# Kernel tuning notes

Measured on AMD Instinct MI355X. Metric: run time of the kernel, lower is better.

Reference implementation:

```python
import jax, jax.numpy as jnp
import numpy as np

DECAY = 0.1
EPS = 1e-5


def setup_inputs() -> dict:
    key = jax.random.key(0)
    k1, k2, k3, k4 = jax.random.split(key, 4)
    N, K, D = 262144, 1024, 64
    x = jax.random.normal(k1, (N, D), dtype=jnp.float32)
    embed = jax.random.normal(k2, (K, D), dtype=jnp.float32) * 0.01
    cluster_size = jax.random.uniform(k3, (K,), dtype=jnp.float32)
    embed_avg = jax.random.normal(k4, (K, D), dtype=jnp.float32) * 0.01
    return {"x": x, "embed": embed, "cluster_size": cluster_size, "embed_avg": embed_avg}


def reference(x, embed, cluster_size, embed_avg):
    # x: [N, D] flattened latents; embed: [K, D] codebook
    N, D = x.shape
    K = embed.shape[0]

    # Squared Euclidean distance (same argmin as torch.cdist p=2).
    x2 = jnp.sum(x * x, axis=-1, keepdims=True)            # [N, 1]
    e2 = jnp.sum(embed * embed, axis=-1)                   # [K]
    dist = x2 - 2.0 * jnp.einsum('nd,kd->nk', x, embed) + e2[None, :]  # [N, K]
    embed_ind = jnp.argmin(dist, axis=-1)                  # [N] int

    # Quantize: gather nearest codes.
    quantize = embed[embed_ind]                            # [N, D]

    # --- EMA codebook update (no-grad in the original) ---
    xs = jax.lax.stop_gradient(x)
    bins = jax.ops.segment_sum(jnp.ones((N,), dtype=x.dtype), embed_ind,
                               num_segments=K)             # [K] bincount
    embed_sum = jax.ops.segment_sum(xs, embed_ind, num_segments=K)  # [K, D] scatter-add

    cluster_size_new = cluster_size * DECAY + bins * (1.0 - DECAY)
    embed_avg_new = embed_avg * DECAY + embed_sum * (1.0 - DECAY)

    # Laplace smoothing then normalize to get the updated codebook.
    n = jnp.sum(cluster_size_new)
    cs_smoothed = (cluster_size_new + EPS) / (n + K * EPS) * n
    embed_normalized = embed_avg_new / cs_smoothed[:, None]  # [K, D]

    return quantize, embed_ind, cluster_size_new, embed_avg_new, embed_normalized
```

## Files before the change

### kernel.cpp

```cpp
#include <hip/hip_runtime.h>
#include <hip/hip_bf16.h>


#define NROWS 262144
#define KCODES 1024
#define DDIM 64
#define CAPL 4

typedef __attribute__((ext_vector_type(8))) short short8;
typedef __attribute__((ext_vector_type(4))) float f32x4;

__device__ __forceinline__ unsigned short f2bf(float f) {
    unsigned u = __float_as_uint(f);
    unsigned r = u + 0x7fffu + ((u >> 16) & 1u);
    return (unsigned short)(r >> 16);
}

__global__ __launch_bounds__(256) void vq_prep(
    const float* __restrict__ embed, unsigned short* __restrict__ eb,
    float* __restrict__ e2f, float* __restrict__ enmax2)
{
    const int k = blockIdx.x * 256 + threadIdx.x;
    const float* er = embed + (size_t)k * DDIM;
    float s = 0.f;
    #pragma unroll
    for (int d = 0; d < DDIM; ++d) { float v = er[d]; s = fmaf(v, v, s); }
    e2f[k] = s;
    unsigned char* base = (unsigned char*)eb + (k >> 8) * 32768 +
                          ((k >> 5) & 7) * 4096 + (k & 31) * 128;
    #pragma unroll
    for (int sl = 0; sl < 8; ++sl) {
        short8 f;
        #pragma unroll
        for (int j = 0; j < 8; ++j) f[j] = (short)f2bf(er[sl * 8 + j]);
        *reinterpret_cast<short8*>(base + ((sl ^ (k & 7)) << 4)) = f;
    }
    atomicMax((int*)enmax2, __float_as_int(s));
}

__global__ __launch_bounds__(512) void vq_phaseA(
    const float* __restrict__ x, const unsigned short* __restrict__ eb,
    const float* __restrict__ e2f, const float* __restrict__ enmax2,
    float* __restrict__ out_ind, int* __restrict__ candg, int* __restrict__ cntg,
    int* __restrict__ wl, int* __restrict__ gcount,
    int* __restrict__ wl2, int* __restrict__ gcount2, int* __restrict__ bins_i)
{
    __shared__ __align__(16) unsigned short ebs0[16384];
    __shared__ __align__(16) unsigned short ebs1[16384];
    __shared__ float e2L[KCODES];
    __shared__ float norm2L[256];
    __shared__ int   cntL[256];
    __shared__ int   candL[256][CAPL];
    __shared__ int   mcount, mbase, mcount2, mbase2;

    const int t    = threadIdx.x;
    const int lane = t & 63;
    const int wid  = t >> 6;
    const int col  = lane & 15;
    const int q    = lane >> 4;
    const int rowb = blockIdx.x * 256;
    const int r0   = wid * 32;

#define STAGEQ(BUF, P)                                                        \
    {                                                                         \
        const unsigned char* gsrc = (const unsigned char*)eb +                \
            (size_t)(P) * 32768 + t * 16;                                     \
        unsigned char* ldst = (unsigned char*)(BUF) + t * 16;                 \
        _Pragma("unroll")                                                     \
        for (int it = 0; it < 4; ++it)                                        \
            __builtin_amdgcn_global_load_lds(                                 \
                (const __attribute__((address_space(1))) void*)(gsrc + it * 8192), \
                (__attribute__((address_space(3))) void*)(ldst + it * 8192),  \
                16, 0, 0);                                                    \
    }

    STAGEQ(ebs0, 0)

    short8 a0[2], a1[2];
    {
        const float* xr = x + (size_t)(rowb + r0 + col) * DDIM;
        float s = 0.f;
        #pragma unroll
        for (int m = 0; m < 2; ++m) {
            const float4 u = *reinterpret_cast<const float4*>(xr + m * 32 + 8 * q);
            const float4 v = *reinterpret_cast<const float4*>(xr + m * 32 + 8 * q + 4);
            short8 f;
            f[0] = (short)f2bf(u.x); f[1] = (short)f2bf(u.y);
            f[2] = (short)f2bf(u.z); f[3] = (short)f2bf(u.w);
            f[4] = (short)f2bf(v.x); f[5] = (short)f2bf(v.y);
            f[6] = (short)f2bf(v.z); f[7] = (short)f2bf(v.w);
            a0[m] = f;
            s = fmaf(u.x, u.x, s); s = fmaf(u.y, u.y, s);
            s = fmaf(u.z, u.z, s); s = fmaf(u.w, u.w, s);
            s = fmaf(v.x, v.x, s); s = fmaf(v.y, v.y, s);
            s = fmaf(v.z, v.z, s); s = fmaf(v.w, v.w, s);
        }
        s += __shfl_xor(s, 16); s += __shfl_xor(s, 32);
        if (lane < 16) norm2L[r0 + lane] = s;
    }
    {
        const float* xr = x + (size_t)(rowb + r0 + 16 + col) * DDIM;
        float s = 0.f;
        #pragma unroll
        for (int m = 0; m < 2; ++m) {
            const float4 u = *reinterpret_cast<const float4*>(xr + m * 32 + 8 * q);
            const float4 v = *reinterpret_cast<const float4*>(xr + m * 32 + 8 * q + 4);
            short8 f;
            f[0] = (short)f2bf(u.x); f[1] = (short)f2bf(u.y);
            f[2] = (short)f2bf(u.z); f[3] = (short)f2bf(u.w);
            f[4] = (short)f2bf(v.x); f[5] = (short)f2bf(v.y);
            f[6] = (short)f2bf(v.z); f[7] = (short)f2bf(v.w);
            a1[m] = f;
            s = fmaf(u.x, u.x, s); s = fmaf(u.y, u.y, s);
            s = fmaf(u.z, u.z, s); s = fmaf(u.w, u.w, s);
            s = fmaf(v.x, v.x, s); s = fmaf(v.y, v.y, s);
            s = fmaf(v.z, v.z, s); s = fmaf(v.w, v.w, s);
        }
        s += __shfl_xor(s, 16); s += __shfl_xor(s, 32);
        if (lane < 16) norm2L[r0 + 16 + lane] = s;
    }

    e2L[t]       = -0.5f * e2f[t];
    e2L[512 + t] = -0.5f * e2f[512 + t];
    if (t < 256) cntL[t] = 0;
    if (t == 0) { mcount = 0; mcount2 = 0; }
    const float en2 = *enmax2;

    const int off0 = col * 128 + ((q       ^ (col & 7)) << 4);
    const int off1 = col * 128 + (((4 + q) ^ (col & 7)) << 4);

    f32x4 best0, best1;
    #pragma unroll
    for (int r = 0; r < 4; ++r) { best0[r] = -3.4e38f; best1[r] = -3.4e38f; }

#define CHUNKS(BUF, P, KIND)                                                  \
    _Pragma("unroll")                                                         \
    for (int ch = 0; ch < 16; ++ch) {                                         \
        const short8 b0 = *reinterpret_cast<const short8*>(                   \
            (char*)(BUF) + ch * 2048 + off0);                                 \
        const short8 b1 = *reinterpret_cast<const short8*>(                   \
            (char*)(BUF) + ch * 2048 + off1);                                 \
        const float e2n = e2L[(P) * 256 + ch * 16 + col];                     \
        f32x4 acc0, acc1;                                                     \
        acc0[0] = e2n; acc0[1] = e2n; acc0[2] = e2n; acc0[3] = e2n;           \
        acc1 = acc0;                                                          \
        acc0 = __builtin_amdgcn_mfma_f32_16x16x32_bf16(a0[0], b0, acc0, 0, 0, 0); \
        acc1 = __builtin_amdgcn_mfma_f32_16x16x32_bf16(a1[0], b0, acc1, 0, 0, 0); \
        acc0 = __builtin_amdgcn_mfma_f32_16x16x32_bf16(a0[1], b1, acc0, 0, 0, 0); \
        acc1 = __builtin_amdgcn_mfma_f32_16x16x32_bf16(a1[1], b1, acc1, 0, 0, 0); \
        if (KIND == 0) {                                                      \
            _Pragma("unroll")                                                 \
            for (int r = 0; r < 4; ++r) {                                     \
                best0[r] = fmaxf(best0[r], acc0[r]);                          \
                best1[r] = fmaxf(best1[r], acc1[r]);                          \
            }                                                                 \
        } else {                                                              \
            _Pragma("unroll")                                                 \
            for (int r = 0; r < 4; ++r) {                                     \
                if (acc0[r] >= best0[r]) {                                    \
                    const int rl = r0 + q * 4 + r;                            \
                    const int idx = atomicAdd(&cntL[rl], 1);                  \
                    if (idx < CAPL) candL[rl][idx] = (P) * 256 + ch * 16 + col; \
                }                                                             \
                if (acc1[r] >= best1[r]) {                                    \
                    const int rl = r0 + 16 + q * 4 + r;                       \
                    const int idx = atomicAdd(&cntL[rl], 1);                  \
                    if (idx < CAPL) candL[rl][idx] = (P) * 256 + ch * 16 + col; \
                }                                                             \
            }                                                                 \
        }                                                                     \
    }

    __syncthreads();
    STAGEQ(ebs1, 1)  CHUNKS(ebs0, 0, 0)  __syncthreads();
    STAGEQ(ebs0, 2)  CHUNKS(ebs1, 1, 0)  __syncthreads();
    STAGEQ(ebs1, 3)  CHUNKS(ebs0, 2, 0)  __syncthreads();
    CHUNKS(ebs1, 3, 0)

    #pragma unroll
    for (int r = 0; r < 4; ++r) {
        float v0 = best0[r], v1 = best1[r];
        v0 = fmaxf(v0, __shfl_xor(v0, 1));  v1 = fmaxf(v1, __shfl_xor(v1, 1));
        v0 = fmaxf(v0, __shfl_xor(v0, 2));  v1 = fmaxf(v1, __shfl_xor(v1, 2));
        v0 = fmaxf(v0, __shfl_xor(v0, 4));  v1 = fmaxf(v1, __shfl_xor(v1, 4));
        v0 = fmaxf(v0, __shfl_xor(v0, 8));  v1 = fmaxf(v1, __shfl_xor(v1, 8));
        const int lr = q * 4 + r;
        const float m0 = 0.0078125f * sqrtf(norm2L[r0 + lr] * en2) + 5e-5f;
        const float m1 = 0.0078125f * sqrtf(norm2L[r0 + 16 + lr] * en2) + 5e-5f;
        best0[r] = v0 - m0;
        best1[r] = v1 - m1;
    }

    STAGEQ(ebs0, 0)  CHUNKS(ebs1, 3, 1)  __syncthreads();
    STAGEQ(ebs1, 1)  CHUNKS(ebs0, 0, 1)  __syncthreads();
    STAGEQ(ebs0, 2)  CHUNKS(ebs1, 1, 1)  __syncthreads();
    CHUNKS(ebs0, 2, 1)
    __syncthreads();

    int my = -1, my2 = -1, c = 0;
    if (t < 256) {
        c = cntL[t];
        if (c == 1) {
            const int code = candL[t][0];
            out_ind[rowb + t] = (float)code;
            atomicAdd(bins_i + code, 1);
        }
        else if (c <= CAPL)   my  = atomicAdd(&mcount, 1);
        else                  my2 = atomicAdd(&mcount2, 1);
    }
    __syncthreads();
    if (t == 0) { mbase = atomicAdd(gcount, mcount); mbase2 = atomicAdd(gcount2, mcount2); }
    __syncthreads();
    if (my >= 0) {
        const int row = rowb + t;
        wl[mbase + my] = row;
        cntg[row] = c;
        #pragma unroll
        for (int j = 0; j < CAPL; ++j)
            if (j < c) candg[row * CAPL + j] = candL[t][j];
    }
    if (my2 >= 0) wl2[mbase2 + my2] = rowb + t;
#undef STAGEQ
#undef CHUNKS
}

__global__ __launch_bounds__(256) void vq_rerank(
    const float* __restrict__ x, const float* __restrict__ embed,
    const float* __restrict__ e2f, const int* __restrict__ wl,
    const int* __restrict__ gcount, const int* __restrict__ cntg,
    const int* __restrict__ candg, const int* __restrict__ wl2,
    const int* __restrict__ gcount2, float* __restrict__ out_ind,
    int* __restrict__ bins_i)
{
    const int t = threadIdx.x;
    const int n = *gcount;
    for (int i = blockIdx.x * 256 + t; i < n; i += gridDim.x * 256) {
        const int row = wl[i];
        float xv[DDIM];
        {
            const float4* xp = reinterpret_cast<const float4*>(x + (size_t)row * DDIM);
            float4 xq[16];
            #pragma unroll
            for (int qq = 0; qq < 16; ++qq) xq[qq] = xp[qq];
            #pragma unroll
            for (int qq = 0; qq < 16; ++qq) {
                xv[qq*4+0] = xq[qq].x; xv[qq*4+1] = xq[qq].y;
                xv[qq*4+2] = xq[qq].z; xv[qq*4+3] = xq[qq].w;
            }
        }
        float x2 = 0.f;
        #pragma unroll
        for (int d = 0; d < DDIM; ++d) x2 = fmaf(xv[d], xv[d], x2);

        const int c = cntg[row];
        float bv = 3.4e38f; int bk = 0x7fffffff;
        for (int ci = 0; ci < c; ++ci) {
            const int k = candg[row * CAPL + ci];
            const float4* ep = reinterpret_cast<const float4*>(embed + (size_t)k * DDIM);
            float dot = 0.f;
            #pragma unroll
            for (int qq = 0; qq < 16; ++qq) {
                const float4 e4 = ep[qq];
                dot = fmaf(xv[qq*4+0], e4.x, dot);
                dot = fmaf(xv[qq*4+1], e4.y, dot);
                dot = fmaf(xv[qq*4+2], e4.z, dot);
                dot = fmaf(xv[qq*4+3], e4.w, dot);
            }
            const float dist = (x2 - 2.0f * dot) + e2f[k];
            if (dist < bv || (dist == bv && k < bk)) { bv = dist; bk = k; }
        }
        out_ind[row] = (float)bk;
        atomicAdd(bins_i + bk, 1);
    }

    const int lane = t & 63;
    const int gw   = (blockIdx.x * 256 + t) >> 6;
    const int nw   = (gridDim.x * 256) >> 6;
    const int n2   = *gcount2;
    for (int e = gw; e < n2; e += nw) {
        const int row = wl2[e];
        float xv[DDIM];
        {
            const float4* xp = reinterpret_cast<const float4*>(x + (size_t)row * DDIM);
            #pragma unroll
            for (int qq = 0; qq < 16; ++qq) {
                const float4 v = xp[qq];
                xv[qq*4+0] = v.x; xv[qq*4+1] = v.y; xv[qq*4+2] = v.z; xv[qq*4+3] = v.w;
            }
        }
        float x2 = 0.f;
        #pragma unroll
        for (int d = 0; d < DDIM; ++d) x2 = fmaf(xv[d], xv[d], x2);

        float bv = 3.4e38f; int bk = 0x7fffffff;
        for (int k = lane; k < KCODES; k += 64) {
            const float* er = embed + (size_t)k * DDIM;
            float dot = 0.f;
            #pragma unroll
            for (int d = 0; d < DDIM; ++d) dot = fmaf(xv[d], er[d], dot);
            const float dist = (x2 - 2.0f * dot) + e2f[k];
            if (dist < bv) { bv = dist; bk = k; }
        }
        #pragma unroll
        for (int s = 1; s < 64; s <<= 1) {
            const float ov = __shfl_xor(bv, s);
            const int   ok = __shfl_xor(bk, s);
            if (ov < bv || (ov == bv && ok < bk)) { bv = ov; bk = ok; }
        }
        if (lane == 0) { out_ind[row] = (float)bk; atomicAdd(bins_i + bk, 1); }
    }
}

__global__ __launch_bounds__(1024) void vq_prefix(
    const int* __restrict__ bins_i, int* __restrict__ cursor)
{
    __shared__ int s[KCODES];
    const int t = threadIdx.x;
    const int b = bins_i[t];
    s[t] = b;
    __syncthreads();
    for (int d = 1; d < KCODES; d <<= 1) {
        const int v = (t >= d) ? s[t - d] : 0;
        __syncthreads();
        s[t] += v;
        __syncthreads();
    }
    cursor[t] = s[t] - b;
}

__global__ __launch_bounds__(256) void vq_scatter(
    const float* __restrict__ out_ind, int* __restrict__ cursor, int* __restrict__ sorted)
{
    const int row  = blockIdx.x * 256 + threadIdx.x;
    const int code = (int)out_ind[row];
    const int pos  = atomicAdd(cursor + code, 1);
    sorted[pos] = (code << 20) | row;
}

__global__ __launch_bounds__(256) void vq_reduce(
    const float* __restrict__ x, const int* __restrict__ sorted,
    float* __restrict__ esum)
{
    const int t = threadIdx.x, lane = t & 63, w = t >> 6;
    const int p0 = (blockIdx.x * 4 + w) * 64;

    int cur = sorted[p0] >> 20;
    float acc = 0.f;
    #pragma unroll 4
    for (int i = 0; i < 64; i += 4) {
        const int4 e4 = *reinterpret_cast<const int4*>(sorted + p0 + i);
        const float v0 = x[(size_t)(e4.x & 0xFFFFF) * DDIM + lane];
        const float v1 = x[(size_t)(e4.y & 0xFFFFF) * DDIM + lane];
        const float v2 = x[(size_t)(e4.z & 0xFFFFF) * DDIM + lane];
        const float v3 = x[(size_t)(e4.w & 0xFFFFF) * DDIM + lane];
        const int c0 = e4.x >> 20, c1 = e4.y >> 20, c2 = e4.z >> 20, c3 = e4.w >> 20;
        if (c0 != cur) { unsafeAtomicAdd(esum + cur * DDIM + lane, acc); acc = 0.f; cur = c0; }
        acc += v0;
        if (c1 != cur) { unsafeAtomicAdd(esum + cur * DDIM + lane, acc); acc = 0.f; cur = c1; }
        acc += v1;
        if (c2 != cur) { unsafeAtomicAdd(esum + cur * DDIM + lane, acc); acc = 0.f; cur = c2; }
        acc += v2;
        if (c3 != cur) { unsafeAtomicAdd(esum + cur * DDIM + lane, acc); acc = 0.f; cur = c3; }
        acc += v3;
    }
    unsafeAtomicAdd(esum + cur * DDIM + lane, acc);
}

__global__ __launch_bounds__(1024) void vq_finalize(
    const float* __restrict__ cluster_size, const float* __restrict__ embed_avg,
    const int* __restrict__ bins_i, float* __restrict__ out_cs,
    float* __restrict__ out_eavg, float* __restrict__ out_enorm)
{
    __shared__ float red[KCODES];
    __shared__ float css[KCODES];
    const int t = threadIdx.x;

    const float csn = cluster_size[t] * 0.1f + (float)bins_i[t] * 0.9f;
    red[t] = csn;
    __syncthreads();
    for (int s = 512; s > 0; s >>= 1) {
        if (t < s) red[t] += red[t + s];
        __syncthreads();
    }
    const float n = red[0];
    out_cs[t] = csn;
    css[t] = (csn + 1e-5f) / (n + (float)(KCODES * 1e-5)) * n;
    __syncthreads();

    #pragma unroll
    for (int i = 0; i < 16; ++i) {
        const int f4 = t + i * 1024;
        const int k  = f4 >> 4;
        const float4 ea = reinterpret_cast<const float4*>(embed_avg)[f4];
        const float4 su = reinterpret_cast<const float4*>(out_eavg)[f4];
        const float  cc = css[k];
        float4 ean, en;
        ean.x = ea.x * 0.1f + su.x * 0.9f; en.x = ean.x / cc;
        ean.y = ea.y * 0.1f + su.y * 0.9f; en.y = ean.y / cc;
        ean.z = ea.z * 0.1f + su.z * 0.9f; en.z = ean.z / cc;
        ean.w = ea.w * 0.1f + su.w * 0.9f; en.w = ean.w / cc;
        reinterpret_cast<float4*>(out_eavg)[f4]  = ean;
        reinterpret_cast<float4*>(out_enorm)[f4] = en;
    }
}

__global__ __launch_bounds__(256) void vq_quant(
    const float* __restrict__ out_ind, const float* __restrict__ embed,
    float* __restrict__ out_q)
{
    __shared__ int inds[256];
    const int t = threadIdx.x;
    const int row0 = blockIdx.x * 256;
    inds[t] = (int)out_ind[row0 + t];
    __syncthreads();
    #pragma unroll
    for (int i = 0; i < 16; ++i) {
        const int f = t + i * 256;
        const int r = f >> 4, dq = f & 15;
        const int code = inds[r];
        const float4 ev = *reinterpret_cast<const float4*>(
            embed + (size_t)code * DDIM + dq * 4);
        *reinterpret_cast<float4*>(out_q + (size_t)(row0 + r) * DDIM + dq * 4) = ev;
    }
}

extern "C" void kernel_launch(void* const* d_in, const int* in_sizes, int n_in,
                              void* d_out, int out_size, void* d_ws, size_t ws_size,
                              hipStream_t stream)
{
    const float* x            = (const float*)d_in[0];
    const float* embed        = (const float*)d_in[1];
    const float* cluster_size = (const float*)d_in[2];
    const float* embed_avg    = (const float*)d_in[3];

    float* out      = (float*)d_out;
    float* out_q    = out;
    float* out_ind  = out_q + (size_t)NROWS * DDIM;
    float* out_cs   = out_ind + NROWS;
    float* out_eavg = out_cs + KCODES;
    float* out_en   = out_eavg + (size_t)KCODES * DDIM;

    unsigned short* eb = (unsigned short*)out_en;
    float* e2f = out_en + 32768;

    int* S      = (int*)out_q;
    int* candg  = S;
    int* cntg   = S + 1048576;
    int* wl     = S + 1310720;
    int* wl2    = S + 1572864;
    int* sorted = S + 1835008;
    int* bins_i = S + 2097152;
    int* gcount = bins_i + KCODES;
    int* gcount2= gcount + 1;
    float* enmax2 = (float*)(gcount2 + 1);
    int* cursor = gcount2 + 2;

    hipMemsetAsync(bins_i, 0, (KCODES + 3) * sizeof(int), stream);
    hipMemsetAsync(out_eavg, 0, (size_t)KCODES * DDIM * sizeof(float), stream);

    vq_prep    <<<KCODES / 256, 256, 0, stream>>>(embed, eb, e2f, enmax2);
    vq_phaseA  <<<NROWS / 256, 512, 0, stream>>>(x, eb, e2f, enmax2, out_ind,
                                                 candg, cntg, wl, gcount,
                                                 wl2, gcount2, bins_i);
    vq_rerank  <<<512, 256, 0, stream>>>(x, embed, e2f, wl, gcount, cntg, candg,
                                         wl2, gcount2, out_ind, bins_i);
    vq_prefix  <<<1, 1024, 0, stream>>>(bins_i, cursor);
    vq_scatter <<<NROWS / 256, 256, 0, stream>>>(out_ind, cursor, sorted);
    vq_reduce  <<<NROWS / 256, 256, 0, stream>>>(x, sorted, out_eavg);
    vq_finalize<<<1, 1024, 0, stream>>>(cluster_size, embed_avg, bins_i,
                                        out_cs, out_eavg, out_en);
    vq_quant   <<<NROWS / 256, 256, 0, stream>>>(out_ind, embed, out_q);
}
```

Baseline: 304.0 us.

## Replace two-pass candidate collection with single-pass running top-3 tracking

The MFMA distance scan no longer makes a second full pass over the codebook to gather near-best candidates. Each lane now keeps a running top-3 (values) with top-2 indices, merges them across lanes with shuffles, and classifies each row as resolved, a two-candidate rerank, or a full fallback. This halves the MFMA and LDS staging work in phase A and simplifies the rerank kernel to exactly two candidates. In exchange it adds per-element select logic and extra registers for the top-3 state, which may lower occupancy, and rows whose third value is within the margin take the full fallback path.

```diff
diff --git a/kernel.cpp b/kernel.cpp
--- a/kernel.cpp
+++ b/kernel.cpp
@@ -5,10 +5,10 @@
 #define NROWS 262144
 #define KCODES 1024
 #define DDIM 64
-#define CAPL 4
 
 typedef __attribute__((ext_vector_type(8))) short short8;
 typedef __attribute__((ext_vector_type(4))) float f32x4;
+typedef __attribute__((ext_vector_type(4))) int   i32x4;
 
 __device__ __forceinline__ unsigned short f2bf(float f) {
     unsigned u = __float_as_uint(f);
@@ -38,10 +38,22 @@
     atomicMax((int*)enmax2, __float_as_int(s));
 }
 
+#define T3U(v, idx, V1, I1, V2, I2, V3)                                       \
+    {                                                                         \
+        const bool g1 = (v) > (V1);                                           \
+        const bool g2 = (v) > (V2);                                           \
+        const bool g3 = (v) > (V3);                                           \
+        (V3) = g2 ? (V2) : (g3 ? (v) : (V3));                                 \
+        (V2) = g1 ? (V1) : (g2 ? (v) : (V2));                                 \
+        (I2) = g1 ? (I1) : (g2 ? (idx) : (I2));                               \
+        (V1) = g1 ? (v) : (V1);                                               \
+        (I1) = g1 ? (idx) : (I1);                                             \
+    }
+
 __global__ __launch_bounds__(512) void vq_phaseA(
     const float* __restrict__ x, const unsigned short* __restrict__ eb,
     const float* __restrict__ e2f, const float* __restrict__ enmax2,
-    float* __restrict__ out_ind, int* __restrict__ candg, int* __restrict__ cntg,
+    float* __restrict__ out_ind, int* __restrict__ candg,
     int* __restrict__ wl, int* __restrict__ gcount,
     int* __restrict__ wl2, int* __restrict__ gcount2, int* __restrict__ bins_i)
 {
@@ -50,7 +62,7 @@
     __shared__ float e2L[KCODES];
     __shared__ float norm2L[256];
     __shared__ int   cntL[256];
-    __shared__ int   candL[256][CAPL];
+    __shared__ int   candL[256][2];
     __shared__ int   mcount, mbase, mcount2, mbase2;
 
     const int t    = threadIdx.x;
@@ -122,19 +134,23 @@
 
     e2L[t]       = -0.5f * e2f[t];
     e2L[512 + t] = -0.5f * e2f[512 + t];
-    if (t < 256) cntL[t] = 0;
     if (t == 0) { mcount = 0; mcount2 = 0; }
     const float en2 = *enmax2;
 
     const int off0 = col * 128 + ((q       ^ (col & 7)) << 4);
     const int off1 = col * 128 + (((4 + q) ^ (col & 7)) << 4);
 
-    f32x4 best0, best1;
-    #pragma unroll
-    for (int r = 0; r < 4; ++r) { best0[r] = -3.4e38f; best1[r] = -3.4e38f; }
-
-#define CHUNKS(BUF, P, KIND)                                                  \
-    _Pragma("unroll")                                                         \
+    f32x4 v1a, v2a, v3a, v1b, v2b, v3b;
+    i32x4 i1a, i2a, i1b, i2b;
+    #pragma unroll
+    for (int r = 0; r < 4; ++r) {
+        v1a[r] = -3.4e38f; v2a[r] = -3.4e38f; v3a[r] = -3.4e38f;
+        v1b[r] = -3.4e38f; v2b[r] = -3.4e38f; v3b[r] = -3.4e38f;
+        i1a[r] = 0; i2a[r] = 0; i1b[r] = 0; i2b[r] = 0;
+    }
+
+#define CHUNKS(BUF, P)                                                        \
+    _Pragma("unroll 4")                                                       \
     for (int ch = 0; ch < 16; ++ch) {                                         \
         const short8 b0 = *reinterpret_cast<const short8*>(                   \
             (char*)(BUF) + ch * 2048 + off0);                                 \
@@ -148,65 +164,69 @@
         acc1 = __builtin_amdgcn_mfma_f32_16x16x32_bf16(a1[0], b0, acc1, 0, 0, 0); \
         acc0 = __builtin_amdgcn_mfma_f32_16x16x32_bf16(a0[1], b1, acc0, 0, 0, 0); \
         acc1 = __builtin_amdgcn_mfma_f32_16x16x32_bf16(a1[1], b1, acc1, 0, 0, 0); \
-        if (KIND == 0) {                                                      \
-            _Pragma("unroll")                                                 \
-            for (int r = 0; r < 4; ++r) {                                     \
-                best0[r] = fmaxf(best0[r], acc0[r]);                          \
-                best1[r] = fmaxf(best1[r], acc1[r]);                          \
-            }                                                                 \
-        } else {                                                              \
-            _Pragma("unroll")                                                 \
-            for (int r = 0; r < 4; ++r) {                                     \
-                if (acc0[r] >= best0[r]) {                                    \
-                    const int rl = r0 + q * 4 + r;                            \
-                    const int idx = atomicAdd(&cntL[rl], 1);                  \
-                    if (idx < CAPL) candL[rl][idx] = (P) * 256 + ch * 16 + col; \
-                }                                                             \
-                if (acc1[r] >= best1[r]) {                                    \
-                    const int rl = r0 + 16 + q * 4 + r;                       \
-                    const int idx = atomicAdd(&cntL[rl], 1);                  \
-                    if (idx < CAPL) candL[rl][idx] = (P) * 256 + ch * 16 + col; \
-                }                                                             \
-            }                                                                 \
+        const int idx = (P) * 256 + ch * 16 + col;                            \
+        _Pragma("unroll")                                                     \
+        for (int r = 0; r < 4; ++r) {                                         \
+            T3U(acc0[r], idx, v1a[r], i1a[r], v2a[r], i2a[r], v3a[r])         \
+            T3U(acc1[r], idx, v1b[r], i1b[r], v2b[r], i2b[r], v3b[r])         \
         }                                                                     \
     }
 
     __syncthreads();
-    STAGEQ(ebs1, 1)  CHUNKS(ebs0, 0, 0)  __syncthreads();
-    STAGEQ(ebs0, 2)  CHUNKS(ebs1, 1, 0)  __syncthreads();
-    STAGEQ(ebs1, 3)  CHUNKS(ebs0, 2, 0)  __syncthreads();
-    CHUNKS(ebs1, 3, 0)
-
-    #pragma unroll
-    for (int r = 0; r < 4; ++r) {
-        float v0 = best0[r], v1 = best1[r];
-        v0 = fmaxf(v0, __shfl_xor(v0, 1));  v1 = fmaxf(v1, __shfl_xor(v1, 1));
-        v0 = fmaxf(v0, __shfl_xor(v0, 2));  v1 = fmaxf(v1, __shfl_xor(v1, 2));
-        v0 = fmaxf(v0, __shfl_xor(v0, 4));  v1 = fmaxf(v1, __shfl_xor(v1, 4));
-        v0 = fmaxf(v0, __shfl_xor(v0, 8));  v1 = fmaxf(v1, __shfl_xor(v1, 8));
-        const int lr = q * 4 + r;
-        const float m0 = 0.0078125f * sqrtf(norm2L[r0 + lr] * en2) + 5e-5f;
-        const float m1 = 0.0078125f * sqrtf(norm2L[r0 + 16 + lr] * en2) + 5e-5f;
-        best0[r] = v0 - m0;
-        best1[r] = v1 - m1;
-    }
-
-    STAGEQ(ebs0, 0)  CHUNKS(ebs1, 3, 1)  __syncthreads();
-    STAGEQ(ebs1, 1)  CHUNKS(ebs0, 0, 1)  __syncthreads();
-    STAGEQ(ebs0, 2)  CHUNKS(ebs1, 1, 1)  __syncthreads();
-    CHUNKS(ebs0, 2, 1)
-    __syncthreads();
-
-    int my = -1, my2 = -1, c = 0;
+    STAGEQ(ebs1, 1)  CHUNKS(ebs0, 0)  __syncthreads();
+    STAGEQ(ebs0, 2)  CHUNKS(ebs1, 1)  __syncthreads();
+    STAGEQ(ebs1, 3)  CHUNKS(ebs0, 2)  __syncthreads();
+    CHUNKS(ebs1, 3)
+
+    #pragma unroll
+    for (int tile = 0; tile < 2; ++tile) {
+        #pragma unroll
+        for (int r = 0; r < 4; ++r) {
+            float a1v = tile ? v1b[r] : v1a[r];
+            float a2v = tile ? v2b[r] : v2a[r];
+            float a3v = tile ? v3b[r] : v3a[r];
+            int   b1v = tile ? i1b[r] : i1a[r];
+            int   b2v = tile ? i2b[r] : i2a[r];
+            #pragma unroll
+            for (int s = 1; s < 16; s <<= 1) {
+                const float w1 = __shfl_xor(a1v, s);
+                const float w2 = __shfl_xor(a2v, s);
+                const float w3 = __shfl_xor(a3v, s);
+                const int   j1 = __shfl_xor(b1v, s);
+                const int   j2 = __shfl_xor(b2v, s);
+                float n1, n2, n3; int m1, m2;
+                if (a1v >= w1) {
+                    n1 = a1v; m1 = b1v;
+                    if (a2v >= w1) { n2 = a2v; m2 = b2v; n3 = fmaxf(a3v, w1); }
+                    else           { n2 = w1;  m2 = j1;  n3 = fmaxf(a2v, w2); }
+                } else {
+                    n1 = w1; m1 = j1;
+                    if (w2 >= a1v) { n2 = w2;  m2 = j2;  n3 = fmaxf(w3, a1v); }
+                    else           { n2 = a1v; m2 = b1v; n3 = fmaxf(w2, a2v); }
+                }
+                a1v = n1; a2v = n2; a3v = n3; b1v = m1; b2v = m2;
+            }
+            if (col == 0) {
+                const int rl = r0 + tile * 16 + q * 4 + r;
+                const float m = 0.0078125f * sqrtf(norm2L[rl] * en2) + 5e-5f;
+                const float thr = a1v - m;
+                cntL[rl] = (a2v < thr) ? 1 : ((a3v < thr) ? 2 : 8);
+                candL[rl][0] = b1v; candL[rl][1] = b2v;
+            }
+        }
+    }
+    __syncthreads();
+
+    int my = -1, my2 = -1;
     if (t < 256) {
-        c = cntL[t];
+        const int c = cntL[t];
         if (c == 1) {
             const int code = candL[t][0];
             out_ind[rowb + t] = (float)code;
             atomicAdd(bins_i + code, 1);
         }
-        else if (c <= CAPL)   my  = atomicAdd(&mcount, 1);
-        else                  my2 = atomicAdd(&mcount2, 1);
+        else if (c == 2)   my  = atomicAdd(&mcount, 1);
+        else               my2 = atomicAdd(&mcount2, 1);
     }
     __syncthreads();
     if (t == 0) { mbase = atomicAdd(gcount, mcount); mbase2 = atomicAdd(gcount2, mcount2); }
@@ -214,10 +234,8 @@
     if (my >= 0) {
         const int row = rowb + t;
         wl[mbase + my] = row;
-        cntg[row] = c;
-        #pragma unroll
-        for (int j = 0; j < CAPL; ++j)
-            if (j < c) candg[row * CAPL + j] = candL[t][j];
+        candg[row * 2 + 0] = candL[t][0];
+        candg[row * 2 + 1] = candL[t][1];
     }
     if (my2 >= 0) wl2[mbase2 + my2] = rowb + t;
 #undef STAGEQ
@@ -227,48 +245,36 @@
 __global__ __launch_bounds__(256) void vq_rerank(
     const float* __restrict__ x, const float* __restrict__ embed,
     const float* __restrict__ e2f, const int* __restrict__ wl,
-    const int* __restrict__ gcount, const int* __restrict__ cntg,
-    const int* __restrict__ candg, const int* __restrict__ wl2,
-    const int* __restrict__ gcount2, float* __restrict__ out_ind,
-    int* __restrict__ bins_i)
+    const int* __restrict__ gcount, const int* __restrict__ candg,
+    const int* __restrict__ wl2, const int* __restrict__ gcount2,
+    float* __restrict__ out_ind, int* __restrict__ bins_i)
 {
     const int t = threadIdx.x;
     const int n = *gcount;
     for (int i = blockIdx.x * 256 + t; i < n; i += gridDim.x * 256) {
         const int row = wl[i];
-        float xv[DDIM];
-        {
-            const float4* xp = reinterpret_cast<const float4*>(x + (size_t)row * DDIM);
-            float4 xq[16];
-            #pragma unroll
-            for (int qq = 0; qq < 16; ++qq) xq[qq] = xp[qq];
-            #pragma unroll
-            for (int qq = 0; qq < 16; ++qq) {
-                xv[qq*4+0] = xq[qq].x; xv[qq*4+1] = xq[qq].y;
-                xv[qq*4+2] = xq[qq].z; xv[qq*4+3] = xq[qq].w;
-            }
-        }
-        float x2 = 0.f;
-        #pragma unroll
-        for (int d = 0; d < DDIM; ++d) x2 = fmaf(xv[d], xv[d], x2);
-
-        const int c = cntg[row];
-        float bv = 3.4e38f; int bk = 0x7fffffff;
-        for (int ci = 0; ci < c; ++ci) {
-            const int k = candg[row * CAPL + ci];
-            const float4* ep = reinterpret_cast<const float4*>(embed + (size_t)k * DDIM);
-            float dot = 0.f;
-            #pragma unroll
-            for (int qq = 0; qq < 16; ++qq) {
-                const float4 e4 = ep[qq];
-                dot = fmaf(xv[qq*4+0], e4.x, dot);
-                dot = fmaf(xv[qq*4+1], e4.y, dot);
-                dot = fmaf(xv[qq*4+2], e4.z, dot);
-                dot = fmaf(xv[qq*4+3], e4.w, dot);
-            }
-            const float dist = (x2 - 2.0f * dot) + e2f[k];
-            if (dist < bv || (dist == bv && k < bk)) { bv = dist; bk = k; }
-        }
+        const int k0 = candg[row * 2 + 0];
+        const int k1 = candg[row * 2 + 1];
+        const float4* xp  = reinterpret_cast<const float4*>(x + (size_t)row * DDIM);
+        const float4* ep0 = reinterpret_cast<const float4*>(embed + (size_t)k0 * DDIM);
+        const float4* ep1 = reinterpret_cast<const float4*>(embed + (size_t)k1 * DDIM);
+        float x2 = 0.f, dot0 = 0.f, dot1 = 0.f;
+        #pragma unroll
+        for (int qq = 0; qq < 16; ++qq) {
+            const float4 xv = xp[qq];
+            const float4 e0 = ep0[qq];
+            const float4 e1 = ep1[qq];
+            x2   = fmaf(xv.x, xv.x, x2);   x2   = fmaf(xv.y, xv.y, x2);
+            x2   = fmaf(xv.z, xv.z, x2);   x2   = fmaf(xv.w, xv.w, x2);
+            dot0 = fmaf(xv.x, e0.x, dot0); dot0 = fmaf(xv.y, e0.y, dot0);
+            dot0 = fmaf(xv.z, e0.z, dot0); dot0 = fmaf(xv.w, e0.w, dot0);
+            dot1 = fmaf(xv.x, e1.x, dot1); dot1 = fmaf(xv.y, e1.y, dot1);
+            dot1 = fmaf(xv.z, e1.z, dot1); dot1 = fmaf(xv.w, e1.w, dot1);
+        }
+        const float d0 = (x2 - 2.0f * dot0) + e2f[k0];
+        const float d1 = (x2 - 2.0f * dot1) + e2f[k1];
+        int bk = k0;
+        if (d1 < d0 || (d1 == d0 && k1 < k0)) bk = k1;
         out_ind[row] = (float)bk;
         atomicAdd(bins_i + bk, 1);
     }
@@ -445,11 +451,10 @@
 
     int* S      = (int*)out_q;
     int* candg  = S;
-    int* cntg   = S + 1048576;
-    int* wl     = S + 1310720;
-    int* wl2    = S + 1572864;
-    int* sorted = S + 1835008;
-    int* bins_i = S + 2097152;
+    int* wl     = S + 524288;
+    int* wl2    = wl + 262144;
+    int* sorted = wl2 + 262144;
+    int* bins_i = sorted + 262144;
     int* gcount = bins_i + KCODES;
     int* gcount2= gcount + 1;
     float* enmax2 = (float*)(gcount2 + 1);
@@ -460,9 +465,9 @@
 
     vq_prep    <<<KCODES / 256, 256, 0, stream>>>(embed, eb, e2f, enmax2);
     vq_phaseA  <<<NROWS / 256, 512, 0, stream>>>(x, eb, e2f, enmax2, out_ind,
-                                                 candg, cntg, wl, gcount,
+                                                 candg, wl, gcount,
                                                  wl2, gcount2, bins_i);
-    vq_rerank  <<<512, 256, 0, stream>>>(x, embed, e2f, wl, gcount, cntg, candg,
+    vq_rerank  <<<512, 256, 0, stream>>>(x, embed, e2f, wl, gcount, candg,
                                          wl2, gcount2, out_ind, bins_i);
     vq_prefix  <<<1, 1024, 0, stream>>>(bins_i, cursor);
     vq_scatter <<<NROWS / 256, 256, 0, stream>>>(out_ind, cursor, sorted);
```

After: 675.4 us. +122.2%, slower.
